# Optimization experiments

Measured on AMD Instinct MI355X. Metric: run time of the kernel, lower is better.

Reference implementation:

```python
import jax, jax.numpy as jnp
import numpy as np

B, N, C = 128, 1024, 1
N_TIMES = 2
NUM_SUBSTEPS = 279  # trunc(dt_Output/dt_sub)+1 for default params


def setup_inputs() -> dict:
    key = jax.random.key(0)
    # small amplitude: d_to_u multiplies spectrum by k (up to N/2), keep CFL stable
    x = jax.random.normal(key, (B, N, C), dtype=jnp.float32) * 1e-3
    return {
        "x": x,
        "nu_para": jnp.float32(-3.0),
        "dt_Output_para": jnp.float32(-3.0),
        "cRatio_para": jnp.float32(0.1),
        "nTimes": N_TIMES,
        "num_substeps": NUM_SUBSTEPS,
    }


def _forward(x, nu_para, dt_Output_para, cRatio_para, nTimes, num_substeps):
    n = x.shape[1]
    L = 2.0 * np.pi
    k = (2.0 * np.pi / L) * jnp.arange(n // 2 + 1, dtype=jnp.float32)  # [n//2+1]
    ik = 1j * k

    # reparameterized physical params (sigmoid squashing, as in the torch module)
    nu = jax.nn.sigmoid(nu_para) * (0.5 - 0.01) + 0.01
    dt_out = jax.nn.sigmoid(dt_Output_para) * (0.1 - 0.001) + 0.001
    cR = jax.nn.sigmoid(cRatio_para) * (2.0 - 0.5) + 0.5

    d = jnp.transpose(x, (0, 2, 1))  # [B, C, N]
    # d_to_u: u = irfft(1j * rfft(d) * k)
    u = jnp.fft.irfft(1j * jnp.fft.rfft(d) * k, n=n)

    dt = dt_out / num_substeps
    # q = 1 - dt*cR*(k + nu*(1j*k)^2) ; (1j*k)^2 = -k^2 so q is real-valued
    q = 1.0 - dt * cR * (k - nu * k * k)

    def substep(u, _):
        uhat = jnp.fft.rfft(u)
        u2hat = jnp.fft.rfft(0.5 * u * u)
        u_new = jnp.fft.irfft((uhat - dt * ik * u2hat) / q, n=n)
        return u_new, None

    def outer(u, _):
        u, _ = jax.lax.scan(substep, u, None, length=num_substeps)
        return u, u

    _, usol = jax.lax.scan(outer, u, None, length=nTimes)  # [T, B, C, N]
    T = usol.shape[0]
    # torch.cat(usol, dim=1): [B, T*C, N] with time-major ordering
    usol = jnp.moveaxis(usol, 0, 1).reshape(usol.shape[1], T * usol.shape[2], n)

    # u_to_d: d_hat = -1j*rfft(u); d_hat[...,1:] /= k[1:]; d_hat[...,0] = 0
    d_hat = -1j * jnp.fft.rfft(usol)
    safe_k = jnp.where(k > 0, k, 1.0)
    d_hat = jnp.where(k > 0, d_hat / safe_k, jnp.zeros((), dtype=d_hat.dtype))
    dsol = jnp.fft.irfft(d_hat, n=n)  # [B, T*C, N]

    return jnp.transpose(dsol, (0, 2, 1))  # [B, N, T*C]


def reference(x, nu_para, dt_Output_para, cRatio_para, nTimes, num_substeps):
    return _forward(x, nu_para, dt_Output_para, cRatio_para, nTimes, num_substeps)
```

## Files before the change

kernel.cpp:

```cpp
#include <hip/hip_runtime.h>
#include <math.h>

#define NFFT 1024
#define BLK  512

template <int CTRL>
__device__ __forceinline__ float dppf(float v) {
    return __int_as_float(__builtin_amdgcn_update_dpp(
        0, __float_as_int(v), CTRL, 0xF, 0xF, true));
}
__device__ __forceinline__ float qx1(float v) { return dppf<0xB1>(v); }
__device__ __forceinline__ float qx2(float v) { return dppf<0x4E>(v); }
__device__ __forceinline__ float qx3(float v) { return dppf<0x1B>(v); }
__device__ __forceinline__ float xr4(float v) { return dppf<0x1B>(dppf<0x141>(v)); }
__device__ __forceinline__ float xr8(float v) { return dppf<0x128>(v); }

__global__ __launch_bounds__(BLK)
void siva_kernel(const float* __restrict__ x,
                 const float* __restrict__ nu_p,
                 const float* __restrict__ dto_p,
                 const float* __restrict__ cr_p,
                 const int* __restrict__ nt_p,
                 const int* __restrict__ ns_p,
                 float* __restrict__ out) {
    __shared__ float2 bufG[NFFT];
    __shared__ float2 bufG2[NFFT];

    const int tt = threadIdx.x;
    const int b  = blockIdx.x;
    const int l  = tt & 63;
    const int w  = tt >> 6;
    const int R = (l >> 4) | (l & 12) | ((l & 3) << 4);

    const int nT   = nt_p[0];
    const int nsub = ns_p[0];

    const float nu  = (1.0f / (1.0f + expf(-nu_p[0])))  * (0.5f - 0.01f)  + 0.01f;
    const float dto = (1.0f / (1.0f + expf(-dto_p[0]))) * (0.1f - 0.001f) + 0.001f;
    const float cR  = (1.0f / (1.0f + expf(-cr_p[0])))  * (2.0f - 0.5f)   + 0.5f;
    const float dt   = dto / (float)nsub;
    const float dtcR = dt * cR;

    float2 T10;
    { const float a = (float)tt * (1.0f / 512.0f);
      T10 = make_float2(cospif(a), -sinpif(a)); }

    float2 E8f[8], D8[8];
    #pragma unroll
    for (int j = 0; j < 8; ++j) {
        const float af = (float)(j * w) * 0.25f + (float)(l * w) * (1.0f / 256.0f);
        E8f[j] = make_float2(cospif(af), -sinpif(af));
        const float ai = (float)(w * j) * 0.25f + (float)(l * j) * (1.0f / 256.0f);
        D8[j] = make_float2(cospif(ai), sinpif(ai));
    }

    float2 GF[3][4], GI[3][4];
    {
        const int hs[3] = {16, 4, 1};
        #pragma unroll
        for (int s = 0; s < 3; ++s) {
            const int h = hs[s];
            const int a = (l / h) & 3;
            const int m = l % h;
            const float invM = 1.0f / (float)(4 * h);
            #pragma unroll
            for (int d = 0; d < 4; ++d) {
                const int e4 = ((d ^ a) * a) & 3;
                const float angF = 0.5f * (float)e4
                                 + 2.0f * (float)(a * m) * invM;
                GF[s][d] = make_float2(cospif(angF), -sinpif(angF));
                const float angI = 0.5f * (float)e4
                                 + 2.0f * (float)((d ^ a) * m) * invM;
                GI[2 - s][d] = make_float2(cospif(angI), sinpif(angI));
            }
        }
    }

    float Sc[2], csn[2], si[2];
    #pragma unroll
    for (int p = 0; p < 2; ++p) {
        const int k = 16 * R + 2 * w + p;
        const float kk = (k <= 512) ? (float)k : (float)(k - 1024);
        const float ka = fabsf(kk);
        const float q  = 1.0f - dtcR * (ka - nu * ka * ka);
        const float a  = (1.0f / q) * (1.0f / 1024.0f);
        const float kkS = (k == 0 || k == 512) ? 0.0f : kk;
        Sc[p]  = a * (1.0f - dt * kkS);
        csn[p] = (k == 0) ? 0.0f : (1.0f / (1024.0f * kk));
        si[p]  = kk * (1.0f / 1024.0f);
    }

    float2 Cf[2][4];
    #pragma unroll
    for (int p = 0; p < 2; ++p) {
        #pragma unroll
        for (int e = 0; e < 4; ++e) {
            float cx = 0.0f, cy = 0.0f;
            #pragma unroll
            for (int d = 0; d < 4; ++d) {
                const float sd = __shfl_xor(Sc[p], d);
                const float gx = __shfl_xor(GF[2][d ^ e].x, d);
                const float gy = __shfl_xor(GF[2][d ^ e].y, d);
                const float2 gi = GI[0][d];
                cx = fmaf(sd, gi.x * gx - gi.y * gy, cx);
                cy = fmaf(sd, gi.x * gy + gi.y * gx, cy);
            }
            Cf[p][e] = make_float2(cx, cy);
        }
    }

    auto c4 = [](float2 g0, float2 z0, float2 g1, float2 z1,
                 float2 g2, float2 z2, float2 g3, float2 z3) -> float2 {
        float xx = g0.x * z0.x;      xx = fmaf(-g0.y, z0.y, xx);
        xx = fmaf(g1.x, z1.x, xx);   xx = fmaf(-g1.y, z1.y, xx);
        xx = fmaf(g2.x, z2.x, xx);   xx = fmaf(-g2.y, z2.y, xx);
        xx = fmaf(g3.x, z3.x, xx);   xx = fmaf(-g3.y, z3.y, xx);
        float yy = g0.x * z0.y;      yy = fmaf(g0.y, z0.x, yy);
        yy = fmaf(g1.x, z1.y, yy);   yy = fmaf(g1.y, z1.x, yy);
        yy = fmaf(g2.x, z2.y, yy);   yy = fmaf(g2.y, z2.x, yy);
        yy = fmaf(g3.x, z3.y, yy);   yy = fmaf(g3.y, z3.x, yy);
        return make_float2(xx, yy);
    };

    auto csum8 = [](const float2* c, const float2* v) -> float2 {
        float xx = c[0].x * v[0].x;  xx = fmaf(-c[0].y, v[0].y, xx);
        float yy = c[0].x * v[0].y;  yy = fmaf(c[0].y, v[0].x, yy);
        #pragma unroll
        for (int j = 1; j < 8; ++j) {
            xx = fmaf(c[j].x, v[j].x, xx);  xx = fmaf(-c[j].y, v[j].y, xx);
            yy = fmaf(c[j].x, v[j].y, yy);  yy = fmaf(c[j].y, v[j].x, yy);
        }
        return make_float2(xx, yy);
    };

    auto stage16 = [&c4](float2 z[2], const float2* G) {
        #pragma unroll
        for (int r = 0; r < 2; ++r) {
            const float2 u1 = make_float2(__shfl_xor(z[r].x, 16), __shfl_xor(z[r].y, 16));
            const float2 u2 = make_float2(__shfl_xor(z[r].x, 32), __shfl_xor(z[r].y, 32));
            const float2 u3 = make_float2(__shfl_xor(z[r].x, 48), __shfl_xor(z[r].y, 48));
            z[r] = c4(G[0], z[r], G[1], u1, G[2], u2, G[3], u3);
        }
    };
    auto stage4dpp = [&c4](float2 z[2], const float2* G) {
        #pragma unroll
        for (int r = 0; r < 2; ++r) {
            const float2 u1 = make_float2(xr4(z[r].x), xr4(z[r].y));
            const float2 u2 = make_float2(xr8(z[r].x), xr8(z[r].y));
            const float2 u3 = make_float2(xr8(u1.x),   xr8(u1.y));
            z[r] = c4(G[0], z[r], G[1], u1, G[2], u2, G[3], u3);
        }
    };
    auto stageQuad = [&c4](float2 z[2], const float2* G) {
        #pragma unroll
        for (int r = 0; r < 2; ++r) {
            const float2 u1 = make_float2(qx1(z[r].x), qx1(z[r].y));
            const float2 u2 = make_float2(qx2(z[r].x), qx2(z[r].y));
            const float2 u3 = make_float2(qx3(z[r].x), qx3(z[r].y));
            z[r] = c4(G[0], z[r], G[1], u1, G[2], u2, G[3], u3);
        }
    };
    auto stageQuadC = [&c4, &Cf](float2 z[2]) {
        #pragma unroll
        for (int p = 0; p < 2; ++p) {
            const float2 u1 = make_float2(qx1(z[p].x), qx1(z[p].y));
            const float2 u2 = make_float2(qx2(z[p].x), qx2(z[p].y));
            const float2 u3 = make_float2(qx3(z[p].x), qx3(z[p].y));
            z[p] = c4(Cf[p][0], z[p], Cf[p][1], u1, Cf[p][2], u2, Cf[p][3], u3);
        }
    };

    auto fwd_head = [&](float2 z[2]) {
        const float2 A  = make_float2(z[0].x + z[1].x, z[0].y + z[1].y);
        const float2 Dm = make_float2(z[0].x - z[1].x, z[0].y - z[1].y);
        const float2 Bc = make_float2(Dm.x * T10.x - Dm.y * T10.y,
                                      Dm.x * T10.y + Dm.y * T10.x);
        bufG[tt] = A;  bufG[512 + tt] = Bc;
        __syncthreads();
        float2 ra[8], rb[8];
        #pragma unroll
        for (int j = 0; j < 8; ++j) {
            ra[j] = bufG[64 * j + l];
            rb[j] = bufG[512 + 64 * j + l];
        }
        z[0] = csum8(E8f, ra);
        z[1] = csum8(E8f, rb);
        stage16(z, GF[0]);
        stage4dpp(z, GF[1]);
    };

    auto inv_tail = [&](float2 z[2], float& u0, float& u1) {
        stage4dpp(z, GI[1]);
        stage16(z, GI[2]);
        bufG2[tt] = z[0];  bufG2[512 + tt] = z[1];
        __syncthreads();
        float2 ya[8], yb[8];
        #pragma unroll
        for (int j = 0; j < 8; ++j) {
            ya[j] = bufG2[64 * j + l];
            yb[j] = bufG2[512 + 64 * j + l];
        }
        const float2 vA = csum8(D8, ya);
        const float2 vB = csum8(D8, yb);
        const float re = vB.x * T10.x + vB.y * T10.y;
        u0 = vA.x + re;
        u1 = vA.x - re;
    };

    float2 z[2];
    float u0, u1;
    z[0] = make_float2(x[b * NFFT + tt], 0.0f);
    z[1] = make_float2(x[b * NFFT + tt + 512], 0.0f);
    fwd_head(z);
    stageQuad(z, GF[2]);
    #pragma unroll
    for (int p = 0; p < 2; ++p) {
        const float zx = z[p].x, zy = z[p].y;
        z[p] = make_float2(-zy * si[p], zx * si[p]);
    }
    stageQuad(z, GI[0]);
    inv_tail(z, u0, u1);

    for (int ot = 0; ot < nT; ++ot) {
        for (int ss = 0; ss < nsub; ++ss) {
            z[0] = make_float2(u0, 0.5f * u0 * u0);
            z[1] = make_float2(u1, 0.5f * u1 * u1);
            fwd_head(z);
            stageQuadC(z);
            inv_tail(z, u0, u1);
        }
        z[0] = make_float2(u0, 0.0f);
        z[1] = make_float2(u1, 0.0f);
        fwd_head(z);
        stageQuad(z, GF[2]);
        #pragma unroll
        for (int p = 0; p < 2; ++p) {
            const float zx = z[p].x, zy = z[p].y;
            z[p] = make_float2(zy * csn[p], -zx * csn[p]);
        }
        stageQuad(z, GI[0]);
        float d0, d1;
        inv_tail(z, d0, d1);
        out[(b * NFFT + tt) * nT + ot]       = d0;
        out[(b * NFFT + tt + 512) * nT + ot] = d1;
    }
}

extern "C" void kernel_launch(void* const* d_in, const int* in_sizes, int n_in,
                              void* d_out, int out_size, void* d_ws, size_t ws_size,
                              hipStream_t stream) {
    const float* x     = (const float*)d_in[0];
    const float* nu_p  = (const float*)d_in[1];
    const float* dto_p = (const float*)d_in[2];
    const float* cr_p  = (const float*)d_in[3];
    const int*   nt_p  = (const int*)d_in[4];
    const int*   ns_p  = (const int*)d_in[5];
    float* out = (float*)d_out;

    const int B = in_sizes[0] / NFFT;
    siva_kernel<<<B, BLK, 0, stream>>>(x, nu_p, dto_p, cr_p, nt_p, ns_p, out);
}
```

Before: 772.7 us.

## Replace radix-4 lane FFT stages with radix-2 butterflies and float4 LDS buffers

Replaces the in-wave radix-4 matrix-style stages (3 stages, each with 3 cross-lane exchanges and 16 FMAs per element) with six radix-2 DIF/DIT butterfly stages using one exchange each. The spectral multiplier is folded into a single radix-2 pair combine (A2/B2). The twiddle tables shrink, and LDS staging is packed into float4 so each thread does one wide store and eight wide loads. The goal is fewer FLOPs and less register pressure in the hot substep loop. The cost is more sequential shuffle/DPP latency from more stages, and bit-reversed ordering must stay consistent.

```diff
diff --git a/kernel.cpp b/kernel.cpp
--- a/kernel.cpp
+++ b/kernel.cpp
@@ -11,7 +11,6 @@
 }
 __device__ __forceinline__ float qx1(float v) { return dppf<0xB1>(v); }
 __device__ __forceinline__ float qx2(float v) { return dppf<0x4E>(v); }
-__device__ __forceinline__ float qx3(float v) { return dppf<0x1B>(v); }
 __device__ __forceinline__ float xr4(float v) { return dppf<0x1B>(dppf<0x141>(v)); }
 __device__ __forceinline__ float xr8(float v) { return dppf<0x128>(v); }
 
@@ -23,14 +22,14 @@
                  const int* __restrict__ nt_p,
                  const int* __restrict__ ns_p,
                  float* __restrict__ out) {
-    __shared__ float2 bufG[NFFT];
-    __shared__ float2 bufG2[NFFT];
+    __shared__ float4 bufF[BLK];
+    __shared__ float4 bufI[BLK];
 
     const int tt = threadIdx.x;
     const int b  = blockIdx.x;
     const int l  = tt & 63;
     const int w  = tt >> 6;
-    const int R = (l >> 4) | (l & 12) | ((l & 3) << 4);
+    const int R  = (int)(__brev((unsigned)l) >> 26);
 
     const int nT   = nt_p[0];
     const int nsub = ns_p[0];
@@ -54,27 +53,24 @@
         D8[j] = make_float2(cospif(ai), sinpif(ai));
     }
 
-    float2 GF[3][4], GI[3][4];
-    {
-        const int hs[3] = {16, 4, 1};
-        #pragma unroll
-        for (int s = 0; s < 3; ++s) {
-            const int h = hs[s];
-            const int a = (l / h) & 3;
-            const int m = l % h;
-            const float invM = 1.0f / (float)(4 * h);
-            #pragma unroll
-            for (int d = 0; d < 4; ++d) {
-                const int e4 = ((d ^ a) * a) & 3;
-                const float angF = 0.5f * (float)e4
-                                 + 2.0f * (float)(a * m) * invM;
-                GF[s][d] = make_float2(cospif(angF), -sinpif(angF));
-                const float angI = 0.5f * (float)e4
-                                 + 2.0f * (float)((d ^ a) * m) * invM;
-                GI[2 - s][d] = make_float2(cospif(angI), sinpif(angI));
-            }
-        }
-    }
+    float2 wf[6]; float sg[6]; float2 wi[6];
+    #pragma unroll
+    for (int s = 0; s < 6; ++s) {
+        const int h = 32 >> s;
+        const int lm = l & (h - 1);
+        const bool hi = (l & h) != 0;
+        const float a = (float)(lm * (32 / h)) * (1.0f / 32.0f);
+        wf[s] = hi ? make_float2(cospif(a), -sinpif(a)) : make_float2(1.0f, 0.0f);
+        sg[s] = hi ? -1.0f : 1.0f;
+        const int h2 = 1 << s;
+        const int lm2 = l & (h2 - 1);
+        const float a2 = (float)lm2 / (float)h2;
+        float2 wb = make_float2(cospif(a2), sinpif(a2));
+        if ((l & h2) != 0) { wb.x = -wb.x; wb.y = -wb.y; }
+        wi[s] = wb;
+    }
+    const bool m2 = (l & 2) != 0, m4 = (l & 4) != 0, m8 = (l & 8) != 0,
+               m16 = (l & 16) != 0, m32 = (l & 32) != 0;
 
     float Sc[2], csn[2], si[2];
     #pragma unroll
@@ -89,85 +85,55 @@
         csn[p] = (k == 0) ? 0.0f : (1.0f / (1024.0f * kk));
         si[p]  = kk * (1.0f / 1024.0f);
     }
-
-    float2 Cf[2][4];
-    #pragma unroll
-    for (int p = 0; p < 2; ++p) {
-        #pragma unroll
-        for (int e = 0; e < 4; ++e) {
-            float cx = 0.0f, cy = 0.0f;
-            #pragma unroll
-            for (int d = 0; d < 4; ++d) {
-                const float sd = __shfl_xor(Sc[p], d);
-                const float gx = __shfl_xor(GF[2][d ^ e].x, d);
-                const float gy = __shfl_xor(GF[2][d ^ e].y, d);
-                const float2 gi = GI[0][d];
-                cx = fmaf(sd, gi.x * gx - gi.y * gy, cx);
-                cy = fmaf(sd, gi.x * gy + gi.y * gx, cy);
-            }
-            Cf[p][e] = make_float2(cx, cy);
-        }
-    }
-
-    auto c4 = [](float2 g0, float2 z0, float2 g1, float2 z1,
-                 float2 g2, float2 z2, float2 g3, float2 z3) -> float2 {
-        float xx = g0.x * z0.x;      xx = fmaf(-g0.y, z0.y, xx);
-        xx = fmaf(g1.x, z1.x, xx);   xx = fmaf(-g1.y, z1.y, xx);
-        xx = fmaf(g2.x, z2.x, xx);   xx = fmaf(-g2.y, z2.y, xx);
-        xx = fmaf(g3.x, z3.x, xx);   xx = fmaf(-g3.y, z3.y, xx);
-        float yy = g0.x * z0.y;      yy = fmaf(g0.y, z0.x, yy);
-        yy = fmaf(g1.x, z1.y, yy);   yy = fmaf(g1.y, z1.x, yy);
-        yy = fmaf(g2.x, z2.y, yy);   yy = fmaf(g2.y, z2.x, yy);
-        yy = fmaf(g3.x, z3.y, yy);   yy = fmaf(g3.y, z3.x, yy);
-        return make_float2(xx, yy);
-    };
-
-    auto csum8 = [](const float2* c, const float2* v) -> float2 {
-        float xx = c[0].x * v[0].x;  xx = fmaf(-c[0].y, v[0].y, xx);
-        float yy = c[0].x * v[0].y;  yy = fmaf(c[0].y, v[0].x, yy);
-        #pragma unroll
-        for (int j = 1; j < 8; ++j) {
-            xx = fmaf(c[j].x, v[j].x, xx);  xx = fmaf(-c[j].y, v[j].y, xx);
-            yy = fmaf(c[j].x, v[j].y, yy);  yy = fmaf(c[j].y, v[j].x, yy);
-        }
-        return make_float2(xx, yy);
-    };
-
-    auto stage16 = [&c4](float2 z[2], const float2* G) {
-        #pragma unroll
-        for (int r = 0; r < 2; ++r) {
-            const float2 u1 = make_float2(__shfl_xor(z[r].x, 16), __shfl_xor(z[r].y, 16));
-            const float2 u2 = make_float2(__shfl_xor(z[r].x, 32), __shfl_xor(z[r].y, 32));
-            const float2 u3 = make_float2(__shfl_xor(z[r].x, 48), __shfl_xor(z[r].y, 48));
-            z[r] = c4(G[0], z[r], G[1], u1, G[2], u2, G[3], u3);
-        }
-    };
-    auto stage4dpp = [&c4](float2 z[2], const float2* G) {
-        #pragma unroll
-        for (int r = 0; r < 2; ++r) {
-            const float2 u1 = make_float2(xr4(z[r].x), xr4(z[r].y));
-            const float2 u2 = make_float2(xr8(z[r].x), xr8(z[r].y));
-            const float2 u3 = make_float2(xr8(u1.x),   xr8(u1.y));
-            z[r] = c4(G[0], z[r], G[1], u1, G[2], u2, G[3], u3);
-        }
-    };
-    auto stageQuad = [&c4](float2 z[2], const float2* G) {
-        #pragma unroll
-        for (int r = 0; r < 2; ++r) {
-            const float2 u1 = make_float2(qx1(z[r].x), qx1(z[r].y));
-            const float2 u2 = make_float2(qx2(z[r].x), qx2(z[r].y));
-            const float2 u3 = make_float2(qx3(z[r].x), qx3(z[r].y));
-            z[r] = c4(G[0], z[r], G[1], u1, G[2], u2, G[3], u3);
-        }
-    };
-    auto stageQuadC = [&c4, &Cf](float2 z[2]) {
-        #pragma unroll
-        for (int p = 0; p < 2; ++p) {
-            const float2 u1 = make_float2(qx1(z[p].x), qx1(z[p].y));
-            const float2 u2 = make_float2(qx2(z[p].x), qx2(z[p].y));
-            const float2 u3 = make_float2(qx3(z[p].x), qx3(z[p].y));
-            z[p] = c4(Cf[p][0], z[p], Cf[p][1], u1, Cf[p][2], u2, Cf[p][3], u3);
-        }
+    float A2[2], B2[2];
+    { const float sg1 = (l & 1) ? -1.0f : 1.0f;
+      #pragma unroll
+      for (int p = 0; p < 2; ++p) {
+          const float so = __shfl_xor(Sc[p], 1);
+          A2[p] = Sc[p] + so;
+          B2[p] = sg1 * (Sc[p] - so);
+      } }
+
+    auto fwd_s = [&](float2& zz, float bx, float by, int s) {
+        const float tx = fmaf(sg[s], zz.x, bx);
+        const float ty = fmaf(sg[s], zz.y, by);
+        zz.x = tx * wf[s].x - ty * wf[s].y;
+        zz.y = tx * wf[s].y + ty * wf[s].x;
+    };
+    auto inv_s = [&](float2& zz, float bx, float by, int s, bool hi) {
+        const float px = hi ? zz.x : bx, py = hi ? zz.y : by;
+        const float qx = hi ? bx : zz.x, qy = hi ? by : zz.y;
+        zz.x = qx + px * wi[s].x - py * wi[s].y;
+        zz.y = qy + px * wi[s].y + py * wi[s].x;
+    };
+
+    auto lane_fwd5 = [&](float2 z[2]) {
+        #pragma unroll
+        for (int r = 0; r < 2; ++r)
+            fwd_s(z[r], __shfl_xor(z[r].x, 32), __shfl_xor(z[r].y, 32), 0);
+        #pragma unroll
+        for (int r = 0; r < 2; ++r)
+            fwd_s(z[r], __shfl_xor(z[r].x, 16), __shfl_xor(z[r].y, 16), 1);
+        #pragma unroll
+        for (int r = 0; r < 2; ++r) fwd_s(z[r], xr8(z[r].x), xr8(z[r].y), 2);
+        #pragma unroll
+        for (int r = 0; r < 2; ++r) fwd_s(z[r], xr4(z[r].x), xr4(z[r].y), 3);
+        #pragma unroll
+        for (int r = 0; r < 2; ++r) fwd_s(z[r], qx2(z[r].x), qx2(z[r].y), 4);
+    };
+    auto lane_inv5 = [&](float2 z[2]) {
+        #pragma unroll
+        for (int r = 0; r < 2; ++r) inv_s(z[r], qx2(z[r].x), qx2(z[r].y), 1, m2);
+        #pragma unroll
+        for (int r = 0; r < 2; ++r) inv_s(z[r], xr4(z[r].x), xr4(z[r].y), 2, m4);
+        #pragma unroll
+        for (int r = 0; r < 2; ++r) inv_s(z[r], xr8(z[r].x), xr8(z[r].y), 3, m8);
+        #pragma unroll
+        for (int r = 0; r < 2; ++r)
+            inv_s(z[r], __shfl_xor(z[r].x, 16), __shfl_xor(z[r].y, 16), 4, m16);
+        #pragma unroll
+        for (int r = 0; r < 2; ++r)
+            inv_s(z[r], __shfl_xor(z[r].x, 32), __shfl_xor(z[r].y, 32), 5, m32);
     };
 
     auto fwd_head = [&](float2 z[2]) {
@@ -175,36 +141,36 @@
         const float2 Dm = make_float2(z[0].x - z[1].x, z[0].y - z[1].y);
         const float2 Bc = make_float2(Dm.x * T10.x - Dm.y * T10.y,
                                       Dm.x * T10.y + Dm.y * T10.x);
-        bufG[tt] = A;  bufG[512 + tt] = Bc;
+        bufF[tt] = make_float4(A.x, A.y, Bc.x, Bc.y);
         __syncthreads();
-        float2 ra[8], rb[8];
+        float2 za = make_float2(0.0f, 0.0f), zb = make_float2(0.0f, 0.0f);
         #pragma unroll
         for (int j = 0; j < 8; ++j) {
-            ra[j] = bufG[64 * j + l];
-            rb[j] = bufG[512 + 64 * j + l];
-        }
-        z[0] = csum8(E8f, ra);
-        z[1] = csum8(E8f, rb);
-        stage16(z, GF[0]);
-        stage4dpp(z, GF[1]);
-    };
-
-    auto inv_tail = [&](float2 z[2], float& u0, float& u1) {
-        stage4dpp(z, GI[1]);
-        stage16(z, GI[2]);
-        bufG2[tt] = z[0];  bufG2[512 + tt] = z[1];
+            const float4 v = bufF[64 * j + l];
+            za.x = fmaf(E8f[j].x, v.x, za.x);  za.x = fmaf(-E8f[j].y, v.y, za.x);
+            za.y = fmaf(E8f[j].x, v.y, za.y);  za.y = fmaf(E8f[j].y, v.x, za.y);
+            zb.x = fmaf(E8f[j].x, v.z, zb.x);  zb.x = fmaf(-E8f[j].y, v.w, zb.x);
+            zb.y = fmaf(E8f[j].x, v.w, zb.y);  zb.y = fmaf(E8f[j].y, v.z, zb.y);
+        }
+        z[0] = za; z[1] = zb;
+        lane_fwd5(z);
+    };
+
+    auto inv_tail = [&](float2 z[2], float& u0o, float& u1o) {
+        lane_inv5(z);
+        bufI[tt] = make_float4(z[0].x, z[0].y, z[1].x, z[1].y);
         __syncthreads();
-        float2 ya[8], yb[8];
+        float vAx = 0.0f, vBx = 0.0f, vBy = 0.0f;
         #pragma unroll
         for (int j = 0; j < 8; ++j) {
-            ya[j] = bufG2[64 * j + l];
-            yb[j] = bufG2[512 + 64 * j + l];
-        }
-        const float2 vA = csum8(D8, ya);
-        const float2 vB = csum8(D8, yb);
-        const float re = vB.x * T10.x + vB.y * T10.y;
-        u0 = vA.x + re;
-        u1 = vA.x - re;
+            const float4 v = bufI[64 * j + l];
+            vAx = fmaf(D8[j].x, v.x, vAx);  vAx = fmaf(-D8[j].y, v.y, vAx);
+            vBx = fmaf(D8[j].x, v.z, vBx);  vBx = fmaf(-D8[j].y, v.w, vBx);
+            vBy = fmaf(D8[j].x, v.w, vBy);  vBy = fmaf(D8[j].y, v.z, vBy);
+        }
+        const float re = vBx * T10.x + vBy * T10.y;
+        u0o = vAx + re;
+        u1o = vAx - re;
     };
 
     float2 z[2];
@@ -212,13 +178,16 @@
     z[0] = make_float2(x[b * NFFT + tt], 0.0f);
     z[1] = make_float2(x[b * NFFT + tt + 512], 0.0f);
     fwd_head(z);
-    stageQuad(z, GF[2]);
+    #pragma unroll
+    for (int r = 0; r < 2; ++r) fwd_s(z[r], qx1(z[r].x), qx1(z[r].y), 5);
     #pragma unroll
     for (int p = 0; p < 2; ++p) {
         const float zx = z[p].x, zy = z[p].y;
         z[p] = make_float2(-zy * si[p], zx * si[p]);
     }
-    stageQuad(z, GI[0]);
+    { const bool m1 = (l & 1) != 0;
+      #pragma unroll
+      for (int r = 0; r < 2; ++r) inv_s(z[r], qx1(z[r].x), qx1(z[r].y), 0, m1); }
     inv_tail(z, u0, u1);
 
     for (int ot = 0; ot < nT; ++ot) {
@@ -226,19 +195,27 @@
             z[0] = make_float2(u0, 0.5f * u0 * u0);
             z[1] = make_float2(u1, 0.5f * u1 * u1);
             fwd_head(z);
-            stageQuadC(z);
+            #pragma unroll
+            for (int p = 0; p < 2; ++p) {
+                const float px = qx1(z[p].x), py = qx1(z[p].y);
+                z[p].x = fmaf(A2[p], z[p].x, B2[p] * px);
+                z[p].y = fmaf(A2[p], z[p].y, B2[p] * py);
+            }
             inv_tail(z, u0, u1);
         }
         z[0] = make_float2(u0, 0.0f);
         z[1] = make_float2(u1, 0.0f);
         fwd_head(z);
-        stageQuad(z, GF[2]);
+        #pragma unroll
+        for (int r = 0; r < 2; ++r) fwd_s(z[r], qx1(z[r].x), qx1(z[r].y), 5);
         #pragma unroll
         for (int p = 0; p < 2; ++p) {
             const float zx = z[p].x, zy = z[p].y;
             z[p] = make_float2(zy * csn[p], -zx * csn[p]);
         }
-        stageQuad(z, GI[0]);
+        { const bool m1 = (l & 1) != 0;
+          #pragma unroll
+          for (int r = 0; r < 2; ++r) inv_s(z[r], qx1(z[r].x), qx1(z[r].y), 0, m1); }
         float d0, d1;
         inv_tail(z, d0, d1);
         out[(b * NFFT + tt) * nT + ot]       = d0;
```

Result: faster. 749.3 us (-3.0%).
